# Optimization experiments

Measured on AMD Instinct MI355X. Metric: run time of the kernel, lower is better.

## Reference

```python
import jax, jax.numpy as jnp
import numpy as np

N_LOW, N_HIGH = 20000, 60000
E_LOW, E_L2H, E_HIGH = 320000, 540000, 480000
EPS = 1e-5
NEG_SLOPE = 0.2


def _gatv2(x_src, x_dst, edge_index, Wl, Wr, att, bias):
    """PyG GATv2Conv with concat heads, aggr='mean', no self loops.
    att: [H, C]. Returns [n_dst, H*C]."""
    H, C = att.shape
    n_dst = x_dst.shape[0]
    xl = (x_src @ Wl).reshape(-1, H, C)   # [n_src, H, C]
    xr = (x_dst @ Wr).reshape(-1, H, C)   # [n_dst, H, C]
    src, dst = edge_index[0], edge_index[1]
    z = jax.nn.leaky_relu(xl[src] + xr[dst], NEG_SLOPE)        # [E, H, C]
    logits = jnp.einsum('ehc,hc->eh', z, att)                  # [E, H]
    m = jax.ops.segment_max(logits, dst, num_segments=n_dst)   # segment softmax
    e = jnp.exp(logits - m[dst])
    s = jax.ops.segment_sum(e, dst, num_segments=n_dst)
    alpha = e / s[dst]                                         # [E, H]
    out = jax.ops.segment_sum(xl[src] * alpha[:, :, None], dst, num_segments=n_dst)
    deg = jax.ops.segment_sum(jnp.ones((src.shape[0],), out.dtype), dst, num_segments=n_dst)
    out = out / jnp.maximum(deg, 1.0)[:, None, None]           # aggr='mean'
    out = out.reshape(n_dst, H * C)
    if bias is not None:
        out = out + bias
    return out


def _bn(x, g, b):
    mu = x.mean(axis=0)
    var = x.var(axis=0)
    return (x - mu) * jax.lax.rsqrt(var + EPS) * g + b


def _forward(x_low, x_high, z_std, e_low, e_l2h, e_high,
             l1_Wl, l1_Wr, l1_att, l1_b, bn1_g, bn1_b,
             l2_Wl, l2_Wr, l2_att, l2_b, bn2_g, bn2_b,
             l3_Wl, l3_Wr, l3_att, l3_b,
             lh_Wl, lh_Wr, lh_att,
             h1_Wl, h1_Wr, h1_att, h1_b, bn3_g, bn3_b,
             h2_Wl, h2_Wr, h2_att, h2_b, bn4_g, bn4_b,
             h3_Wl, h3_Wr, h3_att, h3_b):
    # low_net: GATv2(125->128,h2) -> BN(256) -> GATv2(256->128) -> BN(128) -> GATv2(128->128)
    h = _gatv2(x_low, x_low, e_low, l1_Wl, l1_Wr, l1_att, l1_b)
    h = _bn(h, bn1_g, bn1_b)
    h = _gatv2(h, h, e_low, l2_Wl, l2_Wr, l2_att, l2_b)
    h = _bn(h, bn2_g, bn2_b)
    h = _gatv2(h, h, e_low, l3_Wl, l3_Wr, l3_att, l3_b)
    # bipartite low2high: (encod_low[128], x_high[1]) -> 128, no bias
    eh = _gatv2(h, x_high, e_l2h, lh_Wl, lh_Wr, lh_att, None)
    eh = jnp.concatenate([z_std, eh], axis=-1)                 # [N_HIGH, 129]
    # high_net
    g = _gatv2(eh, eh, e_high, h1_Wl, h1_Wr, h1_att, h1_b)
    g = _bn(g, bn3_g, bn3_b)
    g = _gatv2(g, g, e_high, h2_Wl, h2_Wr, h2_att, h2_b)
    g = _bn(g, bn4_g, bn4_b)
    return _gatv2(g, g, e_high, h3_Wl, h3_Wr, h3_att, h3_b)   # [N_HIGH, 2]


def setup_inputs() -> dict:
    key = jax.random.key(0)
    ks = iter(jax.random.split(key, 64))
    def P(shape, fan_in):
        return jax.random.normal(next(ks), shape, jnp.float32) / np.sqrt(fan_in)
    inp = {}
    inp['x_low'] = jax.random.normal(next(ks), (N_LOW, 125), jnp.float32)
    inp['x_high'] = jax.random.normal(next(ks), (N_HIGH, 1), jnp.float32)
    inp['z_std'] = jax.random.normal(next(ks), (N_HIGH, 1), jnp.float32)
    inp['e_low'] = jnp.stack([jax.random.randint(next(ks), (E_LOW,), 0, N_LOW),
                              jax.random.randint(next(ks), (E_LOW,), 0, N_LOW)])
    inp['e_l2h'] = jnp.stack([jax.random.randint(next(ks), (E_L2H,), 0, N_LOW),
                              jax.random.randint(next(ks), (E_L2H,), 0, N_HIGH)])
    inp['e_high'] = jnp.stack([jax.random.randint(next(ks), (E_HIGH,), 0, N_HIGH),
                               jax.random.randint(next(ks), (E_HIGH,), 0, N_HIGH)])
    inp['l1_Wl'] = P((125, 256), 125); inp['l1_Wr'] = P((125, 256), 125)
    inp['l1_att'] = P((2, 128), 128);  inp['l1_b'] = jnp.zeros((256,), jnp.float32)
    inp['bn1_g'] = jnp.ones((256,), jnp.float32); inp['bn1_b'] = jnp.zeros((256,), jnp.float32)
    inp['l2_Wl'] = P((256, 128), 256); inp['l2_Wr'] = P((256, 128), 256)
    inp['l2_att'] = P((1, 128), 128);  inp['l2_b'] = jnp.zeros((128,), jnp.float32)
    inp['bn2_g'] = jnp.ones((128,), jnp.float32); inp['bn2_b'] = jnp.zeros((128,), jnp.float32)
    inp['l3_Wl'] = P((128, 128), 128); inp['l3_Wr'] = P((128, 128), 128)
    inp['l3_att'] = P((1, 128), 128);  inp['l3_b'] = jnp.zeros((128,), jnp.float32)
    inp['lh_Wl'] = P((128, 128), 128); inp['lh_Wr'] = P((1, 128), 1)
    inp['lh_att'] = P((1, 128), 128)
    inp['h1_Wl'] = P((129, 256), 129); inp['h1_Wr'] = P((129, 256), 129)
    inp['h1_att'] = P((2, 128), 128);  inp['h1_b'] = jnp.zeros((256,), jnp.float32)
    inp['bn3_g'] = jnp.ones((256,), jnp.float32); inp['bn3_b'] = jnp.zeros((256,), jnp.float32)
    inp['h2_Wl'] = P((256, 128), 256); inp['h2_Wr'] = P((256, 128), 256)
    inp['h2_att'] = P((1, 128), 128);  inp['h2_b'] = jnp.zeros((128,), jnp.float32)
    inp['bn4_g'] = jnp.ones((128,), jnp.float32); inp['bn4_b'] = jnp.zeros((128,), jnp.float32)
    inp['h3_Wl'] = P((128, 2), 128);   inp['h3_Wr'] = P((128, 2), 128)
    inp['h3_att'] = P((1, 2), 2);      inp['h3_b'] = jnp.zeros((2,), jnp.float32)
    return inp


def reference(x_low, x_high, z_std, e_low, e_l2h, e_high,
              l1_Wl, l1_Wr, l1_att, l1_b, bn1_g, bn1_b,
              l2_Wl, l2_Wr, l2_att, l2_b, bn2_g, bn2_b,
              l3_Wl, l3_Wr, l3_att, l3_b,
              lh_Wl, lh_Wr, lh_att,
              h1_Wl, h1_Wr, h1_att, h1_b, bn3_g, bn3_b,
              h2_Wl, h2_Wr, h2_att, h2_b, bn4_g, bn4_b,
              h3_Wl, h3_Wr, h3_att, h3_b):
    return _forward(x_low, x_high, z_std, e_low, e_l2h, e_high,
                    l1_Wl, l1_Wr, l1_att, l1_b, bn1_g, bn1_b,
                    l2_Wl, l2_Wr, l2_att, l2_b, bn2_g, bn2_b,
                    l3_Wl, l3_Wr, l3_att, l3_b,
                    lh_Wl, lh_Wr, lh_att,
                    h1_Wl, h1_Wr, h1_att, h1_b, bn3_g, bn3_b,
                    h2_Wl, h2_Wr, h2_att, h2_b, bn4_g, bn4_b,
                    h3_Wl, h3_Wr, h3_att, h3_b)
```

## Files before the change

kernel.cpp:

```cpp
#include <hip/hip_runtime.h>
#include <hip/hip_bf16.h>
#include <cstdint>
#include <cstddef>
#include <cmath>

#define NEG_SLOPE 0.2f

#define PB  1024
#define CSH 10
#define CBS 1024
#define NBCMAX 160
#define PBN 2048

using frag = __attribute__((ext_vector_type(8))) short;
using facc = __attribute__((ext_vector_type(4))) float;

__device__ __forceinline__ float bf_hi(unsigned u) {
    union { unsigned i; float f; } t; t.i = u & 0xffff0000u; return t.f;
}
__device__ __forceinline__ float bf_lo(unsigned u) {
    union { unsigned i; float f; } t; t.i = u << 16; return t.f;
}
__device__ __forceinline__ void unpack8(uint4 u, float* v) {
    v[0] = bf_lo(u.x); v[1] = bf_hi(u.x);
    v[2] = bf_lo(u.y); v[3] = bf_hi(u.y);
    v[4] = bf_lo(u.z); v[5] = bf_hi(u.z);
    v[6] = bf_lo(u.w); v[7] = bf_hi(u.w);
}

typedef const __attribute__((address_space(1))) void* gas_cptr;
typedef __attribute__((address_space(3))) void* las_ptr;
__device__ __forceinline__ void gload_lds16(const __hip_bfloat16* g, __hip_bfloat16* l) {
    __builtin_amdgcn_global_load_lds((gas_cptr)(const void*)g, (las_ptr)(void*)l, 16, 0, 0);
}

__global__ __launch_bounds__(256)
void msplitA(const int* __restrict__ s0, const int* __restrict__ d0, int E0,
             const int* __restrict__ s1, const int* __restrict__ d1, int E1,
             const int* __restrict__ s2, const int* __restrict__ d2, int E2,
             int nc0, int nc1, int nc2, int cap0, int cap1, int cap2,
             int* __restrict__ stage, int* __restrict__ cnt2) {
    __shared__ int hist[NBCMAX];
    __shared__ int rbase[NBCMAX];
    __shared__ int curs[NBCMAX];
    __shared__ int ord[1024];
    __shared__ int obkt[1024];
    const int NBC = nc0 + nc1 + nc2;
    const long Etot = (long)E0 + E1 + E2;
    int tid = threadIdx.x;
    int lane = tid & 63;
    long chunk = (Etot + PB - 1) / PB;
    long c0 = (long)blockIdx.x * chunk;
    long c1 = c0 + chunk; if (c1 > Etot) c1 = Etot;
    const long sec1 = (long)PB * nc0 * cap0;
    const long sec2 = sec1 + (long)PB * nc1 * cap1;
    for (int t = tid; t < NBC; t += 256) curs[t] = 0;
    __syncthreads();
    for (long r0 = c0; r0 < c1; r0 += 1024) {
        int n = (int)((c1 - r0 < 1024) ? (c1 - r0) : 1024);
        for (int t = tid; t < NBC; t += 256) hist[t] = 0;
        __syncthreads();
        int mye[4], myb[4], myr[4];
#pragma unroll
        for (int k = 0; k < 4; ++k) {
            int li = k * 256 + tid;
            myb[k] = -1;
            if (li < n) {
                long i = r0 + li;
                int src, dst, gb;
                if (i < E0) { src = s0[i]; dst = d0[i]; gb = dst >> CSH; }
                else if (i < (long)E0 + E1) { long j = i - E0; src = s1[j]; dst = d1[j]; gb = nc0 + (dst >> CSH); }
                else { long j = i - E0 - E1; src = s2[j]; dst = d2[j]; gb = nc0 + nc1 + (dst >> CSH); }
                mye[k] = (src << CSH) | (dst & (CBS - 1));
                myb[k] = gb;
                myr[k] = atomicAdd(&hist[gb], 1);
            }
        }
        __syncthreads();
        if (tid < 64) {
            int carry = 0;
            for (int base = 0; base < NBC; base += 64) {
                int g = base + lane;
                int v = (g < NBC) ? hist[g] : 0;
                int sum = v;
#pragma unroll
                for (int o = 1; o < 64; o <<= 1) {
                    int t = __shfl_up(sum, o, 64);
                    if (lane >= o) sum += t;
                }
                if (g < NBC) rbase[g] = carry + sum - v;
                carry += __shfl(sum, 63, 64);
            }
        }
        __syncthreads();
#pragma unroll
        for (int k = 0; k < 4; ++k)
            if (myb[k] >= 0) {
                int pos = rbase[myb[k]] + myr[k];
                ord[pos] = mye[k];
                obkt[pos] = myb[k];
            }
        __syncthreads();
        for (int pos = tid; pos < n; pos += 256) {
            int b = obkt[pos];
            int rank = pos - rbase[b] + curs[b];
            long addr; int cap;
            if (b < nc0)            { cap = cap0; addr = (long)(blockIdx.x * nc0 + b) * cap0; }
            else if (b < nc0 + nc1) { cap = cap1; addr = sec1 + (long)(blockIdx.x * nc1 + (b - nc0)) * cap1; }
            else                    { cap = cap2; addr = sec2 + (long)(blockIdx.x * nc2 + (b - nc0 - nc1)) * cap2; }
            if (rank < cap) stage[addr + rank] = ord[pos];
        }
        __syncthreads();
        for (int t = tid; t < NBC; t += 256) curs[t] += hist[t];
        __syncthreads();
    }
    for (int t = tid; t < NBC; t += 256) {
        int cap = (t < nc0) ? cap0 : (t < nc0 + nc1) ? cap1 : cap2;
        int c = curs[t]; if (c > cap) c = cap;
        cnt2[(long)blockIdx.x * NBC + t] = c;
    }
}

__global__ void scanC1(const int* __restrict__ cnt2, int* __restrict__ tot, int NBC) {
    __shared__ int red[256];
    int gb = blockIdx.x;
    int tid = threadIdx.x;
    int s = 0;
    for (int p = tid; p < PB; p += 256) s += cnt2[(long)p * NBC + gb];
    red[tid] = s;
    __syncthreads();
    for (int o = 128; o; o >>= 1) {
        if (tid < o) red[tid] += red[tid + o];
        __syncthreads();
    }
    if (tid == 0) tot[gb] = red[0];
}

__global__ void scanC2(const int* __restrict__ tot, int* __restrict__ cstart,
                       int NBC, int nc0, int nc1) {
    if (threadIdx.x == 0) {
        int c = 0;
        for (int gb = 0; gb < NBC; ++gb) {
            if (gb == nc0 || gb == nc0 + nc1) c = 0;
            cstart[gb] = c;
            c += tot[gb];
        }
    }
}

__global__ __launch_bounds__(1024)
void fineB(const int* __restrict__ cnt2, const int* __restrict__ cstart,
           const int* __restrict__ stage,
           int nc0, int nc1, int nc2, int cap0, int cap1, int cap2,
           int* __restrict__ off0, int* __restrict__ col0, int n0,
           int* __restrict__ off1, int* __restrict__ col1, int n1,
           int* __restrict__ off2, int* __restrict__ col2, int n2) {
    __shared__ int fragb[PB + 1];
    __shared__ int cnt[1024];
    __shared__ int wsum[17];
    const int NBC = nc0 + nc1 + nc2;
    int gb = blockIdx.x;
    int tid = threadIdx.x;
    int lane = tid & 63;
    int wv = tid >> 6;
    int cb, ncg, n; long base2, stride; int* off; int* col;
    const long sec1 = (long)PB * nc0 * cap0;
    const long sec2 = sec1 + (long)PB * nc1 * cap1;
    if (gb < nc0) {
        cb = gb; ncg = nc0; n = n0; off = off0; col = col0;
        base2 = (long)cb * cap0; stride = (long)nc0 * cap0;
    } else if (gb < nc0 + nc1) {
        cb = gb - nc0; ncg = nc1; n = n1; off = off1; col = col1;
        base2 = sec1 + (long)cb * cap1; stride = (long)nc1 * cap1;
    } else {
        cb = gb - nc0 - nc1; ncg = nc2; n = n2; off = off2; col = col2;
        base2 = sec2 + (long)cb * cap2; stride = (long)nc2 * cap2;
    }
    int dlo = cb << CSH;
    int colbase = cstart[gb];
    int v = cnt2[(long)tid * NBC + gb];
    int sum = v;
#pragma unroll
    for (int o = 1; o < 64; o <<= 1) {
        int t = __shfl_up(sum, o, 64);
        if (lane >= o) sum += t;
    }
    if (lane == 63) wsum[wv] = sum;
    __syncthreads();
    if (tid == 0) {
        int c = 0;
        for (int w = 0; w < 16; ++w) { int t = wsum[w]; wsum[w] = c; c += t; }
        wsum[16] = c;
    }
    __syncthreads();
    fragb[tid] = wsum[wv] + sum - v;
    if (tid == 0) fragb[PB] = wsum[16];
    __syncthreads();
    int sz = fragb[PB];
    cnt[tid] = 0;
    __syncthreads();
    for (int p = tid; p < sz; p += 1024) {
        int lo = 0, hi = PB;
        while (hi - lo > 1) { int mid = (lo + hi) >> 1; if (fragb[mid] <= p) lo = mid; else hi = mid; }
        int e = stage[base2 + (long)lo * stride + (p - fragb[lo])];
        atomicAdd(&cnt[e & (CBS - 1)], 1);
    }
    __syncthreads();
    int cv = cnt[tid];
    int csum = cv;
#pragma unroll
    for (int o = 1; o < 64; o <<= 1) {
        int t = __shfl_up(csum, o, 64);
        if (lane >= o) csum += t;
    }
    if (lane == 63) wsum[wv] = csum;
    __syncthreads();
    if (tid == 0) {
        int c = 0;
        for (int w = 0; w < 16; ++w) { int t = wsum[w]; wsum[w] = c; c += t; }
    }
    __syncthreads();
    int excl = wsum[wv] + csum - cv;
    int d = dlo + tid;
    if (d < n) off[d] = colbase + excl;
    if (cb == ncg - 1 && tid == 0) off[n] = colbase + sz;
    __syncthreads();
    cnt[tid] = colbase + excl;
    __syncthreads();
    for (int p = tid; p < sz; p += 1024) {
        int lo = 0, hi = PB;
        while (hi - lo > 1) { int mid = (lo + hi) >> 1; if (fragb[mid] <= p) lo = mid; else hi = mid; }
        int e = stage[base2 + (long)lo * stride + (p - fragb[lo])];
        int pos = atomicAdd(&cnt[e & (CBS - 1)], 1);
        col[pos] = e >> CSH;
    }
}

template<int KP, int KSTEP>
__global__ __launch_bounds__(256)
void gemm_t(const __hip_bfloat16* __restrict__ A,
            const __hip_bfloat16* __restrict__ Bt,
            __hip_bfloat16* __restrict__ C,
            const float* __restrict__ bias, int M, int N) {
    constexpr int CPR = KSTEP / 8;
    constexpr int ITER = CPR / 2;
    __shared__ __hip_bfloat16 As[128 * KSTEP];
    __shared__ __hip_bfloat16 Bs[128 * KSTEP];
    int tid = threadIdx.x;
    int lane = tid & 63;
    int wave = tid >> 6;
    int wm = wave >> 1, wn = wave & 1;
    int quad = lane >> 4, l16 = lane & 15;
    int m0 = blockIdx.y * 128;
    int n0 = blockIdx.x * 128;

    facc acc[4][4] = {};

    for (int k0 = 0; k0 < KP; k0 += KSTEP) {
        if (k0) __syncthreads();
#pragma unroll
        for (int p = 0; p < ITER; ++p) {
            int idx = p * 256 + tid;
            int row = idx / CPR;
            int c = idx - row * CPR;
            int gr = m0 + row; if (gr >= M) gr = M - 1;
            int lbase = (p * 256 + wave * 64) * 8;
            gload_lds16(A + (size_t)gr * KP + k0 + c * 8, As + lbase);
            gload_lds16(Bt + (size_t)(n0 + row) * KP + k0 + c * 8, Bs + lbase);
        }
        __syncthreads();
#pragma unroll
        for (int kk = 0; kk < KSTEP / 32; ++kk) {
            frag a[4], b[4];
#pragma unroll
            for (int i = 0; i < 4; ++i) {
                a[i] = *(const frag*)(As + (wm * 64 + i * 16 + l16) * KSTEP + kk * 32 + quad * 8);
                b[i] = *(const frag*)(Bs + (wn * 64 + i * 16 + l16) * KSTEP + kk * 32 + quad * 8);
            }
#pragma unroll
            for (int i = 0; i < 4; ++i)
#pragma unroll
                for (int j = 0; j < 4; ++j)
                    acc[i][j] = __builtin_amdgcn_mfma_f32_16x16x32_bf16(b[j], a[i], acc[i][j], 0, 0, 0);
        }
    }

    float4 bv[4];
#pragma unroll
    for (int j = 0; j < 4; ++j) {
        int n = n0 + wn * 64 + j * 16 + quad * 4;
        if (bias != nullptr) bv[j] = *(const float4*)(bias + n);
        else { bv[j].x = 0.f; bv[j].y = 0.f; bv[j].z = 0.f; bv[j].w = 0.f; }
    }
#pragma unroll
    for (int i = 0; i < 4; ++i) {
        int m = m0 + wm * 64 + i * 16 + l16;
        if (m >= M) continue;
#pragma unroll
        for (int j = 0; j < 4; ++j) {
            int n = n0 + wn * 64 + j * 16 + quad * 4;
            union { uint2 u; __hip_bfloat16 hh[4]; } pk;
            pk.hh[0] = __float2bfloat16(acc[i][j][0] + bv[j].x);
            pk.hh[1] = __float2bfloat16(acc[i][j][1] + bv[j].y);
            pk.hh[2] = __float2bfloat16(acc[i][j][2] + bv[j].z);
            pk.hh[3] = __float2bfloat16(acc[i][j][3] + bv[j].w);
            *(uint2*)(C + (size_t)m * N + n) = pk.u;
        }
    }
}

__global__ void gemm_n22_bn(const __hip_bfloat16* __restrict__ A,
                            const float* __restrict__ Wl, const float* __restrict__ Wr,
                            const float* __restrict__ s, const float* __restrict__ t,
                            float* __restrict__ YL, float* __restrict__ YR, int M, int K) {
    int i = blockIdx.x * blockDim.x + threadIdx.x;
    if (i >= M) return;
    float l0 = 0.f, l1 = 0.f, r0 = 0.f, r1 = 0.f;
    const unsigned* a = (const unsigned*)(A + (size_t)i * K);
    for (int k2 = 0; k2 < K / 2; ++k2) {
        unsigned u = a[k2];
        int k = k2 * 2;
        float v0 = fmaf(bf_lo(u), s[k], t[k]);
        float v1 = fmaf(bf_hi(u), s[k + 1], t[k + 1]);
        l0 = fmaf(v0, Wl[k * 2 + 0], l0);
        l1 = fmaf(v0, Wl[k * 2 + 1], l1);
        l0 = fmaf(v1, Wl[k * 2 + 2], l0);
        l1 = fmaf(v1, Wl[k * 2 + 3], l1);
        r0 = fmaf(v0, Wr[k * 2 + 0], r0);
        r1 = fmaf(v0, Wr[k * 2 + 1], r1);
        r0 = fmaf(v1, Wr[k * 2 + 2], r0);
        r1 = fmaf(v1, Wr[k * 2 + 3], r1);
    }
    YL[(size_t)i * 2 + 0] = l0;
    YL[(size_t)i * 2 + 1] = l1;
    YR[(size_t)i * 2 + 0] = r0;
    YR[(size_t)i * 2 + 1] = r1;
}

__global__ void prep_all(const float* __restrict__ l1Wl, const float* __restrict__ l1Wr,
                         const float* __restrict__ lhWl,
                         const float* __restrict__ h1Wl, const float* __restrict__ h1Wr,
                         const float* __restrict__ x_low, const float* __restrict__ x_high,
                         const float* __restrict__ lhWr, const float* __restrict__ z_std,
                         __hip_bfloat16* __restrict__ w_l1, __hip_bfloat16* __restrict__ w_lh,
                         __hip_bfloat16* __restrict__ w_h1,
                         __hip_bfloat16* __restrict__ XLOWB, __hip_bfloat16* __restrict__ XRo,
                         __hip_bfloat16* __restrict__ EHB,
                         int o1, int o2, int o3, int o4, int o5, int o6, int o7, int o8) {
    int i = blockIdx.x * blockDim.x + threadIdx.x;
    if (i < o1) {
        int r = i >> 7, c = i & 127;
        XLOWB[i] = __float2bfloat16((c < 125) ? x_low[(size_t)r * 125 + c] : 0.f);
    } else if (i < o2) {
        int j = i - o1; int r = j >> 7, c = j & 127;
        XRo[j] = __float2bfloat16(x_high[r] * lhWr[c]);
    } else if (i < o3) {
        int j = i - o2; int r = j >> 5, c = (j & 31) + 128;
        EHB[(size_t)r * 160 + c] = __float2bfloat16((c == 128) ? z_std[r] : 0.f);
    } else if (i < o4) {
        int j = i - o3; int n = j >> 7, k = j & 127;
        w_l1[j] = __float2bfloat16((k < 125) ? l1Wl[(size_t)k * 256 + n] : 0.f);
    } else if (i < o5) {
        int j = i - o4; int n = j >> 7, k = j & 127;
        w_l1[256 * 128 + j] = __float2bfloat16((k < 125) ? l1Wr[(size_t)k * 256 + n] : 0.f);
    } else if (i < o6) {
        int j = i - o5; int n = j >> 7, k = j & 127;
        w_lh[j] = __float2bfloat16(lhWl[(size_t)k * 128 + n]);
    } else if (i < o7) {
        int j = i - o6; int n = j / 160, k = j - n * 160;
        float v = 0.f;
        if (k < 128) v = h1Wl[(size_t)(k + 1) * 256 + n];
        else if (k == 128) v = h1Wl[n];
        w_h1[j] = __float2bfloat16(v);
    } else if (i < o8) {
        int j = i - o7; int n = j / 160, k = j - n * 160;
        float v = 0.f;
        if (k < 128) v = h1Wr[(size_t)(k + 1) * 256 + n];
        else if (k == 128) v = h1Wr[n];
        w_h1[256 * 160 + j] = __float2bfloat16(v);
    }
}

__global__ void wconv_bnfold2(const float* __restrict__ Wl, const float* __restrict__ Wr,
                              const float* __restrict__ scale, const float* __restrict__ shift,
                              __hip_bfloat16* __restrict__ Wt, float* __restrict__ bout,
                              int K, int N, int Kp) {
    __shared__ float red[256];
    const float* W = blockIdx.y ? Wr : Wl;
    __hip_bfloat16* wt = Wt + (size_t)blockIdx.y * N * Kp;
    float* bo = bout + blockIdx.y * N;
    int n = blockIdx.x;
    int tid = threadIdx.x;
    float acc = 0.f;
    for (int k = tid; k < Kp; k += 256) {
        float v = 0.f;
        if (k < K) {
            float w = W[(size_t)k * N + n];
            v = w * scale[k];
            acc = fmaf(w, shift[k], acc);
        }
        wt[(size_t)n * Kp + k] = __float2bfloat16(v);
    }
    red[tid] = acc;
    __syncthreads();
    for (int o = 128; o; o >>= 1) {
        if (tid < o) red[tid] += red[tid + o];
        __syncthreads();
    }
    if (tid == 0) bo[n] = red[0];
}

__global__ void gat_c128_v4(const __hip_bfloat16* __restrict__ xl, int xls,
                            const __hip_bfloat16* __restrict__ xr, int xrs,
                            const int* __restrict__ row_off, const int* __restrict__ col,
                            const float* __restrict__ att, const float* __restrict__ bias,
                            __hip_bfloat16* __restrict__ outb, int obstride,
                            int n_dst, int H) {
    int wid = (blockIdx.x * blockDim.x + threadIdx.x) >> 6;
    int lane = threadIdx.x & 63;
    int total = n_dst * H;
    if (wid >= total) return;
    int dst = wid / H;
    int h = wid - dst * H;
    int g = lane >> 4;
    int q = lane & 15;
    int cb = h * 128 + q * 8;
    int beg = row_off[dst], end = row_off[dst + 1];

    float xrv[8], av[8];
    unpack8(*(const uint4*)(xr + (size_t)dst * xrs + cb), xrv);
    {
        float4 a0 = *(const float4*)(att + cb);
        float4 a1 = *(const float4*)(att + cb + 4);
        av[0] = a0.x; av[1] = a0.y; av[2] = a0.z; av[3] = a0.w;
        av[4] = a1.x; av[5] = a1.y; av[6] = a1.z; av[7] = a1.w;
    }

    float s = 0.f;
    float acc[8] = {0.f, 0.f, 0.f, 0.f, 0.f, 0.f, 0.f, 0.f};

    if (beg < end) {
        int e0g = beg + g;
        bool pv = e0g < end;
        int i0 = col[pv ? e0g : beg];
        uint4 u = *(const uint4*)(xl + (size_t)i0 * xls + cb);
        int e1g = beg + 4 + g;
        int i1 = (beg + 4 < end) ? col[(e1g < end) ? e1g : beg] : 0;

        for (int e0 = beg; e0 < end; e0 += 4) {
            bool have_next = (e0 + 4) < end;
            uint4 un;
            if (have_next)
                un = *(const uint4*)(xl + (size_t)i1 * xls + cb);
            int e2g = e0 + 8 + g;
            int i2 = (e0 + 8 < end) ? col[(e2g < end) ? e2g : beg] : 0;
            bool nv = (e0 + 4 + g) < end;

            float v[8];
            unpack8(u, v);
            float p = 0.f;
#pragma unroll
            for (int c = 0; c < 8; ++c) {
                float z = v[c] + xrv[c];
                z = fmaxf(z, NEG_SLOPE * z);
                p = fmaf(z, av[c], p);
            }
            p += __shfl_xor(p, 8, 64);
            p += __shfl_xor(p, 4, 64);
            p += __shfl_xor(p, 2, 64);
            p += __shfl_xor(p, 1, 64);
            if (!pv) p = -INFINITY;
            float w = __expf(fminf(p, 85.f));
            s += w;
#pragma unroll
            for (int c = 0; c < 8; ++c) acc[c] = fmaf(w, v[c], acc[c]);

            if (have_next) { u = un; pv = nv; }
            i1 = i2;
        }
    }

#pragma unroll
    for (int o = 16; o <= 32; o <<= 1) {
        s += __shfl_xor(s, o, 64);
#pragma unroll
        for (int c = 0; c < 8; ++c) acc[c] += __shfl_xor(acc[c], o, 64);
    }

    int deg = end - beg;
    float inv = (deg > 0) ? 1.f / (s * (float)deg) : 0.f;
    float o8[8];
#pragma unroll
    for (int c = 0; c < 8; ++c) o8[c] = acc[c] * inv;
    if (bias != nullptr) {
#pragma unroll
        for (int c = 0; c < 8; ++c) o8[c] += bias[cb + c];
    }
    if (g == 0) {
        union { uint4 u; __hip_bfloat16 hh[8]; } pk;
#pragma unroll
        for (int c = 0; c < 8; ++c) pk.hh[c] = __float2bfloat16(o8[c]);
        *(uint4*)(outb + (size_t)dst * obstride + cb) = pk.u;
    }
}

__global__ void gat_c256h2(const __hip_bfloat16* __restrict__ xl, int xls,
                           const __hip_bfloat16* __restrict__ xr, int xrs,
                           const int* __restrict__ row_off, const int* __restrict__ col,
                           const float* __restrict__ att, const float* __restrict__ bias,
                           __hip_bfloat16* __restrict__ outb, int obstride,
                           int n_dst) {
    int dst = (blockIdx.x * blockDim.x + threadIdx.x) >> 6;
    int lane = threadIdx.x & 63;
    if (dst >= n_dst) return;
    int g = lane >> 5;
    int q = lane & 31;
    int cb = q * 8;
    int beg = row_off[dst], end = row_off[dst + 1];

    float xrv[8], av[8];
    unpack8(*(const uint4*)(xr + (size_t)dst * xrs + cb), xrv);
    {
        float4 a0 = *(const float4*)(att + cb);
        float4 a1 = *(const float4*)(att + cb + 4);
        av[0] = a0.x; av[1] = a0.y; av[2] = a0.z; av[3] = a0.w;
        av[4] = a1.x; av[5] = a1.y; av[6] = a1.z; av[7] = a1.w;
    }

    float s = 0.f;
    float acc[8] = {0.f, 0.f, 0.f, 0.f, 0.f, 0.f, 0.f, 0.f};

    if (beg < end) {
        int e0g = beg + g;
        bool pv = e0g < end;
        int i0 = col[pv ? e0g : beg];
        uint4 u = *(const uint4*)(xl + (size_t)i0 * xls + cb);
        int e1g = beg + 2 + g;
        int i1 = (beg + 2 < end) ? col[(e1g < end) ? e1g : beg] : 0;

        for (int e0 = beg; e0 < end; e0 += 2) {
            bool have_next = (e0 + 2) < end;
            uint4 un;
            if (have_next)
                un = *(const uint4*)(xl + (size_t)i1 * xls + cb);
            int e2g = e0 + 4 + g;
            int i2 = (e0 + 4 < end) ? col[(e2g < end) ? e2g : beg] : 0;
            bool nv = (e0 + 2 + g) < end;

            float v[8];
            unpack8(u, v);
            float p = 0.f;
#pragma unroll
            for (int c = 0; c < 8; ++c) {
                float z = v[c] + xrv[c];
                z = fmaxf(z, NEG_SLOPE * z);
                p = fmaf(z, av[c], p);
            }
            p += __shfl_xor(p, 8, 64);
            p += __shfl_xor(p, 4, 64);
            p += __shfl_xor(p, 2, 64);
            p += __shfl_xor(p, 1, 64);
            if (!pv) p = -INFINITY;
            float w = __expf(fminf(p, 85.f));
            s += w;
#pragma unroll
            for (int c = 0; c < 8; ++c) acc[c] = fmaf(w, v[c], acc[c]);

            if (have_next) { u = un; pv = nv; }
            i1 = i2;
        }
    }

    s += __shfl_xor(s, 32, 64);
#pragma unroll
    for (int c = 0; c < 8; ++c) acc[c] += __shfl_xor(acc[c], 32, 64);

    int deg = end - beg;
    float inv = (deg > 0) ? 1.f / (s * (float)deg) : 0.f;
    float o8[8];
#pragma unroll
    for (int c = 0; c < 8; ++c) o8[c] = acc[c] * inv;
    if (bias != nullptr) {
#pragma unroll
        for (int c = 0; c < 8; ++c) o8[c] += bias[cb + c];
    }
    if (g == 0) {
        union { uint4 u; __hip_bfloat16 hh[8]; } pk;
#pragma unroll
        for (int c = 0; c < 8; ++c) pk.hh[c] = __float2bfloat16(o8[c]);
        *(uint4*)(outb + (size_t)dst * obstride + cb) = pk.u;
    }
}

__global__ void gat_c2(const float* __restrict__ xl, const float* __restrict__ xr,
                       const int* __restrict__ row_off, const int* __restrict__ col,
                       const float* __restrict__ att, const float* __restrict__ bias,
                       float* __restrict__ out, int n_dst) {
    int dst = blockIdx.x * blockDim.x + threadIdx.x;
    if (dst >= n_dst) return;
    float x0 = xr[(size_t)dst * 2], x1 = xr[(size_t)dst * 2 + 1];
    float a0 = att[0], a1 = att[1];
    int beg = row_off[dst], end = row_off[dst + 1];
    float s = 0.f, acc0 = 0.f, acc1 = 0.f;
    for (int e = beg; e < end; ++e) {
        int src = col[e];
        float v0 = xl[(size_t)src * 2], v1 = xl[(size_t)src * 2 + 1];
        float z0 = v0 + x0; z0 = fmaxf(z0, NEG_SLOPE * z0);
        float z1 = v1 + x1; z1 = fmaxf(z1, NEG_SLOPE * z1);
        float p = fmaf(z0, a0, z1 * a1);
        float w = __expf(fminf(p, 85.f));
        s += w;
        acc0 = fmaf(w, v0, acc0);
        acc1 = fmaf(w, v1, acc1);
    }
    int deg = end - beg;
    float o0 = 0.f, o1 = 0.f;
    if (deg > 0) {
        float inv = 1.f / (s * (float)deg);
        o0 = acc0 * inv;
        o1 = acc1 * inv;
    }
    out[(size_t)dst * 2 + 0] = o0 + bias[0];
    out[(size_t)dst * 2 + 1] = o1 + bias[1];
}

__global__ void bn_partial_d(const __hip_bfloat16* __restrict__ x, float* __restrict__ part,
                             int Nr, int rpb) {
    int C = blockDim.x;
    int c = threadIdx.x;
    int b = blockIdx.x;
    int r0 = b * rpb;
    int r1 = r0 + rpb; if (r1 > Nr) r1 = Nr;
    float s = 0.f, q = 0.f;
    for (int r = r0; r < r1; ++r) {
        float v = __bfloat162float(x[(size_t)r * C + c]);
        s += v;
        q = fmaf(v, v, q);
    }
    part[(size_t)b * C + c] = s;
    part[(size_t)PBN * 256 + (size_t)b * C + c] = q;
}

__global__ void bn_finalize_w(const float* __restrict__ part,
                              const float* __restrict__ g, const float* __restrict__ b,
                              float* __restrict__ scale, float* __restrict__ shift,
                              int Nr, int C) {
    int c = (blockIdx.x * blockDim.x + threadIdx.x) >> 6;
    int lane = threadIdx.x & 63;
    if (c >= C) return;
    float s = 0.f, q = 0.f;
    for (int blk = lane; blk < PBN; blk += 64) {
        s += part[(size_t)blk * C + c];
        q += part[(size_t)PBN * 256 + (size_t)blk * C + c];
    }
#pragma unroll
    for (int o = 32; o; o >>= 1) {
        s += __shfl_xor(s, o, 64);
        q += __shfl_xor(q, o, 64);
    }
    if (lane == 0) {
        float mu = s / (float)Nr;
        float var = q / (float)Nr - mu * mu;
        float inv = rsqrtf(var + 1e-5f);
        float a = g[c] * inv;
        scale[c] = a;
        shift[c] = b[c] - mu * a;
    }
}

extern "C" void kernel_launch(void* const* d_in, const int* in_sizes, int n_in,
                              void* d_out, int out_size, void* d_ws, size_t ws_size,
                              hipStream_t stream) {
    const float* x_low  = (const float*)d_in[0];
    const float* x_high = (const float*)d_in[1];
    const float* z_std  = (const float*)d_in[2];
    const int* e_low  = (const int*)d_in[3];
    const int* e_l2h  = (const int*)d_in[4];
    const int* e_high = (const int*)d_in[5];
    const float* l1_Wl = (const float*)d_in[6];
    const float* l1_Wr = (const float*)d_in[7];
    const float* l1_att = (const float*)d_in[8];
    const float* l1_b  = (const float*)d_in[9];
    const float* bn1_g = (const float*)d_in[10];
    const float* bn1_b = (const float*)d_in[11];
    const float* l2_Wl = (const float*)d_in[12];
    const float* l2_Wr = (const float*)d_in[13];
    const float* l2_att = (const float*)d_in[14];
    const float* l2_b  = (const float*)d_in[15];
    const float* bn2_g = (const float*)d_in[16];
    const float* bn2_b = (const float*)d_in[17];
    const float* l3_Wl = (const float*)d_in[18];
    const float* l3_Wr = (const float*)d_in[19];
    const float* l3_att = (const float*)d_in[20];
    const float* l3_b  = (const float*)d_in[21];
    const float* lh_Wl = (const float*)d_in[22];
    const float* lh_Wr = (const float*)d_in[23];
    const float* lh_att = (const float*)d_in[24];
    const float* h1_Wl = (const float*)d_in[25];
    const float* h1_Wr = (const float*)d_in[26];
    const float* h1_att = (const float*)d_in[27];
    const float* h1_b  = (const float*)d_in[28];
    const float* bn3_g = (const float*)d_in[29];
    const float* bn3_b = (const float*)d_in[30];
    const float* h2_Wl = (const float*)d_in[31];
    const float* h2_Wr = (const float*)d_in[32];
    const float* h2_att = (const float*)d_in[33];
    const float* h2_b  = (const float*)d_in[34];
    const float* bn4_g = (const float*)d_in[35];
    const float* bn4_b = (const float*)d_in[36];
    const float* h3_Wl = (const float*)d_in[37];
    const float* h3_Wr = (const float*)d_in[38];
    const float* h3_att = (const float*)d_in[39];
    const float* h3_b  = (const float*)d_in[40];

    const int N_low = in_sizes[0] / 125;
    const int N_high = in_sizes[1];
    const int E_low = in_sizes[3] / 2;
    const int E_l2h = in_sizes[4] / 2;
    const int E_high = in_sizes[5] / 2;

    char* ws = (char*)d_ws;
    size_t woff = 0;
    auto walloc = [&](size_t bytes) -> void* {
        void* p = (void*)(ws + woff);
        woff += (bytes + 255) & ~(size_t)255;
        return p;
    };
    __hip_bfloat16* XLR = (__hip_bfloat16*)walloc((size_t)N_high * 512 * 2);
    __hip_bfloat16* A1  = (__hip_bfloat16*)walloc((size_t)N_high * 256 * 2);
    __hip_bfloat16* A2  = (__hip_bfloat16*)walloc((size_t)N_high * 128 * 2);
    __hip_bfloat16* XRo = (__hip_bfloat16*)walloc((size_t)N_high * 128 * 2);
    __hip_bfloat16* XLOWB = (__hip_bfloat16*)walloc((size_t)N_low * 128 * 2);
    __hip_bfloat16* EHB = (__hip_bfloat16*)walloc((size_t)N_high * 160 * 2);
    float* YL = (float*)walloc((size_t)N_high * 2 * 4);
    float* YR = (float*)walloc((size_t)N_high * 2 * 4);
    int* off_low  = (int*)walloc((size_t)(N_low + 1) * 4);
    int* col_low  = (int*)walloc((size_t)E_low * 4);
    int* off_l2h  = (int*)walloc((size_t)(N_high + 1) * 4);
    int* col_l2h  = (int*)walloc((size_t)E_l2h * 4);
    int* off_high = (int*)walloc((size_t)(N_high + 1) * 4);
    int* col_high = (int*)walloc((size_t)E_high * 4);
    const int nc0 = (N_low + CBS - 1) >> CSH;
    const int nc1 = (N_high + CBS - 1) >> CSH;
    const int nc2 = (N_high + CBS - 1) >> CSH;
    const int NBC = nc0 + nc1 + nc2;
    const long Etot = (long)E_low + E_l2h + E_high;
    const long chunk = (Etot + PB - 1) / PB;
    auto capf = [&](int ng) {
        double m = (double)chunk * CBS / ng;
        int c = (int)(m + 8.0 * sqrt(m) + 16.0);
        return (c + 15) & ~15;
    };
    const int cap0 = capf(N_low);
    const int cap1 = capf(N_high);
    const int cap2 = capf(N_high);
    int* cnt2   = (int*)walloc((size_t)PB * NBC * 4);
    int* cstart = (int*)walloc((size_t)(NBC + 1) * 4);
    int* ctot   = (int*)walloc((size_t)(NBC + 1) * 4);
    float* bnpart = (float*)walloc((size_t)2 * PBN * 256 * 4);
    float* bnsc   = (float*)walloc(512 * 4);
    float* bb     = (float*)walloc(512 * 4);
    __hip_bfloat16* w_l1 = (__hip_bfloat16*)walloc(512 * 128 * 2);
    __hip_bfloat16* w_l2 = (__hip_bfloat16*)walloc(256 * 256 * 2);
    __hip_bfloat16* w_l3 = (__hip_bfloat16*)walloc(256 * 128 * 2);
    __hip_bfloat16* w_lh = (__hip_bfloat16*)walloc(128 * 128 * 2);
    __hip_bfloat16* w_h1 = (__hip_bfloat16*)walloc(512 * 160 * 2);
    __hip_bfloat16* w_h2 = (__hip_bfloat16*)walloc(256 * 256 * 2);

    int* stage = (int*)XLR;

    {
        int o1 = N_low * 128;
        int o2 = o1 + N_high * 128;
        int o3 = o2 + N_high * 32;
        int o4 = o3 + 256 * 128;
        int o5 = o4 + 256 * 128;
        int o6 = o5 + 128 * 128;
        int o7 = o6 + 256 * 160;
        int o8 = o7 + 256 * 160;
        prep_all<<<(o8 + 255) / 256, 256, 0, stream>>>(
            l1_Wl, l1_Wr, lh_Wl, h1_Wl, h1_Wr, x_low, x_high, lh_Wr, z_std,
            w_l1, w_lh, w_h1, XLOWB, XRo, EHB,
            o1, o2, o3, o4, o5, o6, o7, o8);
    }

    msplitA<<<PB, 256, 0, stream>>>(
        e_low, e_low + E_low, E_low,
        e_l2h, e_l2h + E_l2h, E_l2h,
        e_high, e_high + E_high, E_high,
        nc0, nc1, nc2, cap0, cap1, cap2, stage, cnt2);
    scanC1<<<NBC, 256, 0, stream>>>(cnt2, ctot, NBC);
    scanC2<<<1, 64, 0, stream>>>(ctot, cstart, NBC, nc0, nc1);
    fineB<<<NBC, 1024, 0, stream>>>(cnt2, cstart, stage,
                                    nc0, nc1, nc2, cap0, cap1, cap2,
                                    off_low, col_low, N_low,
                                    off_l2h, col_l2h, N_high,
                                    off_high, col_high, N_high);

    auto gemm = [&](const __hip_bfloat16* A, const __hip_bfloat16* Bt, __hip_bfloat16* C,
                    int M, int N, int Kp, const float* bias) {
        dim3 g(N / 128, (M + 127) / 128);
        if (Kp == 128)      gemm_t<128, 128><<<g, 256, 0, stream>>>(A, Bt, C, bias, M, N);
        else if (Kp == 160) gemm_t<160, 160><<<g, 256, 0, stream>>>(A, Bt, C, bias, M, N);
        else                gemm_t<256, 128><<<g, 256, 0, stream>>>(A, Bt, C, bias, M, N);
    };
    auto gat1 = [&](const __hip_bfloat16* xl, int xls, const __hip_bfloat16* xr, int xrs,
                    const int* roff, const int* colv,
                    const float* att, const float* bias,
                    __hip_bfloat16* outb, int obs, int n_dst) {
        long thr = (long)n_dst * 64;
        gat_c128_v4<<<(unsigned)((thr + 255) / 256), 256, 0, stream>>>(
            xl, xls, xr, xrs, roff, colv, att, bias, outb, obs, n_dst, 1);
    };
    auto gat2 = [&](const __hip_bfloat16* xl, int xls, const __hip_bfloat16* xr, int xrs,
                    const int* roff, const int* colv,
                    const float* att, const float* bias,
                    __hip_bfloat16* outb, int obs, int n_dst) {
        long thr = (long)n_dst * 64;
        gat_c256h2<<<(unsigned)((thr + 255) / 256), 256, 0, stream>>>(
            xl, xls, xr, xrs, roff, colv, att, bias, outb, obs, n_dst);
    };
    auto bn_stats = [&](__hip_bfloat16* x, const float* g, const float* b, int Nr, int C) {
        int rpb = (Nr + PBN - 1) / PBN;
        bn_partial_d<<<PBN, C, 0, stream>>>(x, bnpart, Nr, rpb);
        bn_finalize_w<<<(C * 64 + 255) / 256, 256, 0, stream>>>(bnpart, g, b, bnsc, bnsc + 256, Nr, C);
    };
    auto fold2 = [&](const float* Wl, const float* Wr, __hip_bfloat16* Wt,
                     int K, int Nn, int Kp) {
        dim3 g(Nn, 2);
        wconv_bnfold2<<<g, 256, 0, stream>>>(Wl, Wr, bnsc, bnsc + 256, Wt, bb, K, Nn, Kp);
    };

    gemm(XLOWB, w_l1, XLR, N_low, 512, 128, nullptr);
    gat2(XLR, 512, XLR + 256, 512, off_low, col_low, l1_att, l1_b, A1, 256, N_low);
    bn_stats(A1, bn1_g, bn1_b, N_low, 256);

    fold2(l2_Wl, l2_Wr, w_l2, 256, 128, 256);
    gemm(A1, w_l2, XLR, N_low, 256, 256, bb);
    gat1(XLR, 256, XLR + 128, 256, off_low, col_low, l2_att, l2_b, A2, 128, N_low);
    bn_stats(A2, bn2_g, bn2_b, N_low, 128);

    fold2(l3_Wl, l3_Wr, w_l3, 128, 128, 128);
    gemm(A2, w_l3, XLR, N_low, 256, 128, bb);
    gat1(XLR, 256, XLR + 128, 256, off_low, col_low, l3_att, l3_b, A1, 128, N_low);

    gemm(A1, w_lh, XLR, N_low, 128, 128, nullptr);
    gat1(XLR, 128, XRo, 128, off_l2h, col_l2h, lh_att, nullptr, EHB, 160, N_high);

    gemm(EHB, w_h1, XLR, N_high, 512, 160, nullptr);
    gat2(XLR, 512, XLR + 256, 512, off_high, col_high, h1_att, h1_b, A1, 256, N_high);
    bn_stats(A1, bn3_g, bn3_b, N_high, 256);

    fold2(h2_Wl, h2_Wr, w_h2, 256, 128, 256);
    gemm(A1, w_h2, XLR, N_high, 256, 256, bb);
    gat1(XLR, 256, XLR + 128, 256, off_high, col_high, h2_att, h2_b, A2, 128, N_high);
    bn_stats(A2, bn4_g, bn4_b, N_high, 128);

    gemm_n22_bn<<<(N_high + 255) / 256, 256, 0, stream>>>(A2, h3_Wl, h3_Wr,
                                                          bnsc, bnsc + 256, YL, YR, N_high, 128);
    gat_c2<<<(N_high + 255) / 256, 256, 0, stream>>>(YL, YR, off_high, col_high,
                                                     h3_att, h3_b, (float*)d_out, N_high);
}
```

Baseline: 611.7 us.

## Pack two destinations per wave in C128 GAT and deepen C256 prefetch

The 128-channel GATv2 aggregation kernel now maps two destination nodes onto one wavefront, 32 lanes each, processing two edges per step. The loop runs to the larger of the two degrees and masks lanes past their own degree. This halves the wave count and cuts the cross-lane reduction to one shuffle round, at the cost of idle lanes when the paired degrees differ. The 256-channel, two-head kernel gets a two-stage feature prefetch (u0/u1/u2) so more gather latency is hidden, at the cost of extra registers.

```diff
diff --git a/kernel.cpp b/kernel.cpp
--- a/kernel.cpp
+++ b/kernel.cpp
@@ -410,25 +410,27 @@
     if (tid == 0) bo[n] = red[0];
 }
 
-__global__ void gat_c128_v4(const __hip_bfloat16* __restrict__ xl, int xls,
+__global__ void gat_c128_p2(const __hip_bfloat16* __restrict__ xl, int xls,
                             const __hip_bfloat16* __restrict__ xr, int xrs,
                             const int* __restrict__ row_off, const int* __restrict__ col,
                             const float* __restrict__ att, const float* __restrict__ bias,
                             __hip_bfloat16* __restrict__ outb, int obstride,
-                            int n_dst, int H) {
-    int wid = (blockIdx.x * blockDim.x + threadIdx.x) >> 6;
+                            int n_dst) {
+    int pair = (blockIdx.x * blockDim.x + threadIdx.x) >> 6;
     int lane = threadIdx.x & 63;
-    int total = n_dst * H;
-    if (wid >= total) return;
-    int dst = wid / H;
-    int h = wid - dst * H;
-    int g = lane >> 4;
+    int d = pair * 2 + (lane >> 5);
+    int g = (lane >> 4) & 1;
     int q = lane & 15;
-    int cb = h * 128 + q * 8;
-    int beg = row_off[dst], end = row_off[dst + 1];
+    int cb = q * 8;
+    bool dvalid = d < n_dst;
+    int dd = dvalid ? d : (n_dst - 1);
+    int beg = row_off[dd], end = row_off[dd + 1];
+    int deg = dvalid ? (end - beg) : 0;
+    int md = deg;
+    md = max(md, __shfl_xor(md, 32, 64));
 
     float xrv[8], av[8];
-    unpack8(*(const uint4*)(xr + (size_t)dst * xrs + cb), xrv);
+    unpack8(*(const uint4*)(xr + (size_t)dd * xrs + cb), xrv);
     {
         float4 a0 = *(const float4*)(att + cb);
         float4 a1 = *(const float4*)(att + cb + 4);
@@ -439,22 +441,21 @@
     float s = 0.f;
     float acc[8] = {0.f, 0.f, 0.f, 0.f, 0.f, 0.f, 0.f, 0.f};
 
-    if (beg < end) {
-        int e0g = beg + g;
-        bool pv = e0g < end;
-        int i0 = col[pv ? e0g : beg];
+    if (md > 0) {
+        bool pv = (g) < deg;
+        int i0 = pv ? col[beg + g] : 0;
         uint4 u = *(const uint4*)(xl + (size_t)i0 * xls + cb);
-        int e1g = beg + 4 + g;
-        int i1 = (beg + 4 < end) ? col[(e1g < end) ? e1g : beg] : 0;
-
-        for (int e0 = beg; e0 < end; e0 += 4) {
-            bool have_next = (e0 + 4) < end;
+        int i1 = 0;
+        if (2 < md) { bool p1 = (2 + g) < deg; i1 = p1 ? col[beg + 2 + g] : 0; }
+
+        for (int e = 0; e < md; e += 2) {
+            bool have_next = (e + 2) < md;
             uint4 un;
             if (have_next)
                 un = *(const uint4*)(xl + (size_t)i1 * xls + cb);
-            int e2g = e0 + 8 + g;
-            int i2 = (e0 + 8 < end) ? col[(e2g < end) ? e2g : beg] : 0;
-            bool nv = (e0 + 4 + g) < end;
+            int i2 = 0;
+            if (e + 4 < md) { bool p2 = (e + 4 + g) < deg; i2 = p2 ? col[beg + e + 4 + g] : 0; }
+            bool nv = (e + 2 + g) < deg;
 
             float v[8];
             unpack8(u, v);
@@ -480,14 +481,10 @@
         }
     }
 
-#pragma unroll
-    for (int o = 16; o <= 32; o <<= 1) {
-        s += __shfl_xor(s, o, 64);
-#pragma unroll
-        for (int c = 0; c < 8; ++c) acc[c] += __shfl_xor(acc[c], o, 64);
-    }
-
-    int deg = end - beg;
+    s += __shfl_xor(s, 16, 64);
+#pragma unroll
+    for (int c = 0; c < 8; ++c) acc[c] += __shfl_xor(acc[c], 16, 64);
+
     float inv = (deg > 0) ? 1.f / (s * (float)deg) : 0.f;
     float o8[8];
 #pragma unroll
@@ -496,11 +493,11 @@
 #pragma unroll
         for (int c = 0; c < 8; ++c) o8[c] += bias[cb + c];
     }
-    if (g == 0) {
+    if (g == 0 && dvalid) {
         union { uint4 u; __hip_bfloat16 hh[8]; } pk;
 #pragma unroll
         for (int c = 0; c < 8; ++c) pk.hh[c] = __float2bfloat16(o8[c]);
-        *(uint4*)(outb + (size_t)dst * obstride + cb) = pk.u;
+        *(uint4*)(outb + (size_t)d * obstride + cb) = pk.u;
     }
 }
 
@@ -517,6 +514,7 @@
     int q = lane & 31;
     int cb = q * 8;
     int beg = row_off[dst], end = row_off[dst + 1];
+    int deg = end - beg;
 
     float xrv[8], av[8];
     unpack8(*(const uint4*)(xr + (size_t)dst * xrs + cb), xrv);
@@ -530,25 +528,28 @@
     float s = 0.f;
     float acc[8] = {0.f, 0.f, 0.f, 0.f, 0.f, 0.f, 0.f, 0.f};
 
-    if (beg < end) {
-        int e0g = beg + g;
-        bool pv = e0g < end;
-        int i0 = col[pv ? e0g : beg];
-        uint4 u = *(const uint4*)(xl + (size_t)i0 * xls + cb);
-        int e1g = beg + 2 + g;
-        int i1 = (beg + 2 < end) ? col[(e1g < end) ? e1g : beg] : 0;
-
-        for (int e0 = beg; e0 < end; e0 += 2) {
-            bool have_next = (e0 + 2) < end;
-            uint4 un;
-            if (have_next)
-                un = *(const uint4*)(xl + (size_t)i1 * xls + cb);
-            int e2g = e0 + 4 + g;
-            int i2 = (e0 + 4 < end) ? col[(e2g < end) ? e2g : beg] : 0;
-            bool nv = (e0 + 2 + g) < end;
+    if (deg > 0) {
+        bool pv0 = g < deg;
+        int i0 = col[pv0 ? beg + g : beg];
+        uint4 u0 = *(const uint4*)(xl + (size_t)i0 * xls + cb);
+        bool pv1 = (2 + g) < deg;
+        uint4 u1;
+        if (2 < deg) {
+            int i1 = col[pv1 ? beg + 2 + g : beg];
+            u1 = *(const uint4*)(xl + (size_t)i1 * xls + cb);
+        }
+        int i2 = (4 < deg) ? col[((4 + g) < deg) ? beg + 4 + g : beg] : 0;
+
+        for (int e = 0; e < deg; e += 2) {
+            bool has2 = (e + 4) < deg;
+            uint4 u2;
+            if (has2)
+                u2 = *(const uint4*)(xl + (size_t)i2 * xls + cb);
+            int i3 = ((e + 6) < deg) ? col[((e + 6 + g) < deg) ? beg + e + 6 + g : beg] : 0;
+            bool pv2 = (e + 4 + g) < deg;
 
             float v[8];
-            unpack8(u, v);
+            unpack8(u0, v);
             float p = 0.f;
 #pragma unroll
             for (int c = 0; c < 8; ++c) {
@@ -560,14 +561,15 @@
             p += __shfl_xor(p, 4, 64);
             p += __shfl_xor(p, 2, 64);
             p += __shfl_xor(p, 1, 64);
-            if (!pv) p = -INFINITY;
+            if (!pv0) p = -INFINITY;
             float w = __expf(fminf(p, 85.f));
             s += w;
 #pragma unroll
             for (int c = 0; c < 8; ++c) acc[c] = fmaf(w, v[c], acc[c]);
 
-            if (have_next) { u = un; pv = nv; }
-            i1 = i2;
+            u0 = u1; pv0 = pv1;
+            u1 = u2; pv1 = pv2;
+            i2 = i3;
         }
     }
 
@@ -575,7 +577,6 @@
 #pragma unroll
     for (int c = 0; c < 8; ++c) acc[c] += __shfl_xor(acc[c], 32, 64);
 
-    int deg = end - beg;
     float inv = (deg > 0) ? 1.f / (s * (float)deg) : 0.f;
     float o8[8];
 #pragma unroll
@@ -808,9 +809,10 @@
                     const int* roff, const int* colv,
                     const float* att, const float* bias,
                     __hip_bfloat16* outb, int obs, int n_dst) {
-        long thr = (long)n_dst * 64;
-        gat_c128_v4<<<(unsigned)((thr + 255) / 256), 256, 0, stream>>>(
-            xl, xls, xr, xrs, roff, colv, att, bias, outb, obs, n_dst, 1);
+        long waves = (n_dst + 1) / 2;
+        long thr = waves * 64;
+        gat_c128_p2<<<(unsigned)((thr + 255) / 256), 256, 0, stream>>>(
+            xl, xls, xr, xrs, roff, colv, att, bias, outb, obs, n_dst);
     };
     auto gat2 = [&](const __hip_bfloat16* xl, int xls, const __hip_bfloat16* xr, int xrs,
                     const int* roff, const int* colv,
```

After: 616.5 us. About the same (+0.8%).
